# Performance work log

Measured on AMD Instinct MI355X. Metric: run time of the kernel, lower is better.

## Reference

```python
import jax, jax.numpy as jnp
import numpy as np

B, T, C, H = 256, 256, 384, 6
HS = C // H        # 64 head size
P = int(C * 0.8)   # 307 pca_dim
EPS = 1e-6


def _rmsnorm(x, scale):
    rms = jnp.sqrt(jnp.mean(x * x, axis=-1, keepdims=True) + EPS)
    return x / rms * scale


def _orth(W):
    # torch.svd returns V (not V^T); u @ v.t() == u @ vt
    u, _, vt = jnp.linalg.svd(W, full_matrices=False)
    return u @ vt


def setup_inputs() -> dict:
    key = jax.random.key(0)
    ks = jax.random.split(key, 16)
    s = 0.02
    inp = {
        'x': jax.random.normal(ks[0], (B, T, C), jnp.float32),
        'Wq': jax.random.normal(ks[1], (H, C, HS), jnp.float32) * s,
        'Wk': jax.random.normal(ks[2], (H, C, HS), jnp.float32) * s,
        'Wv': jax.random.normal(ks[3], (H, C, HS), jnp.float32) * s,
        'Wp': jax.random.normal(ks[4], (H * HS, C), jnp.float32) * s,
        'bp': jnp.zeros((C,), jnp.float32),
        'scale1': jnp.ones((C,), jnp.float32),
        'scale2': jnp.ones((C,), jnp.float32),
        'W1': jax.random.normal(ks[5], (C, P), jnp.float32) * s,
        'b1': jnp.zeros((P,), jnp.float32),
        'W2': jax.random.normal(ks[6], (P, C), jnp.float32) * s,
        'b2': jnp.zeros((C,), jnp.float32),
        'Wo_in': jax.random.normal(ks[7], (C, C), jnp.float32),
        'Wo_out': jax.random.normal(ks[8], (C, C), jnp.float32),
    }
    return inp


def reference(x, Wq, Wk, Wv, Wp, bp, scale1, scale2, W1, b1, W2, b2, Wo_in, Wo_out):
    # ln1
    h = _rmsnorm(x, scale1)                                   # [B,T,C]
    # multi-head causal self-attention (heads batched via einsum)
    q = jnp.einsum('btc,hcd->bhtd', h, Wq)                    # [B,H,T,HS]
    k = jnp.einsum('btc,hcd->bhtd', h, Wk)
    v = jnp.einsum('btc,hcd->bhtd', h, Wv)
    wei = jnp.einsum('bhtd,bhsd->bhts', q, k) * (HS ** -0.5)  # [B,H,T,T]
    causal = jnp.tril(jnp.ones((T, T), bool))
    wei = jnp.where(causal, wei, -jnp.inf)
    wei = jax.nn.softmax(wei, axis=-1)
    attn = jnp.einsum('bhts,bhsd->bhtd', wei, v)              # [B,H,T,HS]
    attn = attn.transpose(0, 2, 1, 3).reshape(B, T, H * HS)   # concat heads
    h = attn @ Wp + bp + h                                    # residual on ln1 output
    # ln2
    h = _rmsnorm(h, scale2)
    # input orthogonal transform
    h = h @ _orth(Wo_in)
    # PCA feed-forward (dropout = identity in eval)
    h = jax.nn.relu(h @ W1 + b1)
    h = h @ W2 + b2
    # output orthogonal transform + residual on ff output
    out = h @ _orth(Wo_out) + h
    return out
```

## Files before the change

kernel.cpp:

```cpp
#include <hip/hip_runtime.h>

typedef unsigned short u16;
typedef unsigned int   u32;
typedef short s16x8 __attribute__((ext_vector_type(8)));
typedef float f32x4 __attribute__((ext_vector_type(4)));

static __device__ __forceinline__ float bf2f(u16 v){ return __uint_as_float(((u32)v)<<16); }
static __device__ __forceinline__ u16 f2bf(float f){
  u32 u = __float_as_uint(f);
  u32 r = (u + 0x7fffu + ((u>>16)&1u)) >> 16;
  return (u16)r;
}
static __device__ __forceinline__ float cvt(float v){ return v; }
static __device__ __forceinline__ float cvt(u16 v){ return bf2f(v); }
static __device__ __forceinline__ void stv(float* p, float v){ *p = v; }
static __device__ __forceinline__ void stv(u16* p, float v){ *p = f2bf(v); }

static __device__ __forceinline__ void ld2(const float* p, float& a, float& b){
  float2 t = *(const float2*)p; a=t.x; b=t.y;
}
static __device__ __forceinline__ void ld2(const u16* p, float& a, float& b){
  u32 t = *(const u32*)p; a = __uint_as_float(t<<16); b = __uint_as_float(t & 0xffff0000u);
}
static __device__ __forceinline__ void st2(float* p, float a, float b){
  float2 t; t.x=a; t.y=b; *(float2*)p = t;
}
static __device__ __forceinline__ void st2(u16* p, float a, float b){
  *(u32*)p = ((u32)f2bf(a)) | (((u32)f2bf(b))<<16);
}

static __device__ __forceinline__ void gload16(const u16* g, u16* l){
  __builtin_amdgcn_global_load_lds(
      (const __attribute__((address_space(1))) u32*)(const void*)g,
      (__attribute__((address_space(3))) u32*)(void*)l, 16, 0, 0);
}

template<typename TI, typename TO>
__global__ __launch_bounds__(256) void rms_k(const TI* __restrict__ X,
                                             const float* __restrict__ scale,
                                             TO* __restrict__ O)
{
  int row = blockIdx.x*4 + (threadIdx.x>>6);
  int lane = threadIdx.x&63;
  const TI* xr = X + (size_t)row*384;
  float v[6]; float ss = 0.f;
#pragma unroll
  for(int i=0;i<3;i++){
    ld2(xr + 2*lane + 128*i, v[2*i], v[2*i+1]);
    ss += v[2*i]*v[2*i] + v[2*i+1]*v[2*i+1];
  }
#pragma unroll
  for(int off=32; off>0; off>>=1) ss += __shfl_down(ss, off, 64);
  ss = __shfl(ss, 0, 64);
  float r = rsqrtf(ss*(1.0f/384.0f)+1e-6f);
  TO* orow = O + (size_t)row*384;
#pragma unroll
  for(int i=0;i<3;i++){
    int c = 2*lane + 128*i;
    st2(orow + c, v[2*i]*r*scale[c], v[2*i+1]*r*scale[c+1]);
  }
}

__global__ __launch_bounds__(256) void tcast_k(const float* __restrict__ In, long isz,
                                               u16* __restrict__ Out, long osz,
                                               int Rr, int Cc, int ldo)
{
  __shared__ float t[32][33];
  const int z = blockIdx.z;
  const float* I = In + (long)z*isz;
  u16* Oz = Out + (long)z*osz;
  const int r0 = blockIdx.x*32, c0 = blockIdx.y*32;
  const int tx = threadIdx.x&31, ty = threadIdx.x>>5;
#pragma unroll
  for(int rr=ty; rr<32; rr+=8){
    int r = r0+rr, c = c0+tx;
    t[rr][tx] = (r<Rr && c<Cc) ? I[(size_t)r*Cc + c] : 0.f;
  }
  __syncthreads();
#pragma unroll
  for(int cc=ty; cc<32; cc+=8){
    int c = c0+cc, r = r0+tx;
    if(c<Cc && r<ldo) Oz[(size_t)c*ldo + r] = f2bf(t[tx][cc]);
  }
}

template<int NF, typename TC, typename TR>
__global__ __launch_bounds__(256,3) void mgemm2_k(
    const u16* __restrict__ A, int lda,
    const u16* __restrict__ Bt, int ldb,
    TC* __restrict__ C, long cs_hi, int cs_lo, int csz,
    const TR* __restrict__ R,
    const float* __restrict__ bias,
    int N, int Nstore, int K, float beta, int relu, int nby)
{
  constexpr int BN = NF*32;
  __shared__ __align__(16) u16 As[128*64];
  __shared__ __align__(16) u16 Bs[BN*64];
  const int d = blockIdx.x;
  const int xcd = d&7, slot = d>>3;
  const int bm = xcd*64 + slot/nby;
  const int bn = slot - (slot/nby)*nby;
  const int m0 = bm*128, n0 = bn*BN;
  const int tid = threadIdx.x;
  const int w = tid>>6, lane = tid&63;
  const int g4 = lane>>4, l16 = lane&15;
  const int wr = w>>1, wc = w&1;
  const int srow = lane>>3;
  const int sc8  = ((lane&7) ^ srow) * 8;
  const u16* aSrc[4];
#pragma unroll
  for(int i=0;i<4;i++)
    aSrc[i] = A + (size_t)(m0 + 8*(w+4*i) + srow)*lda + sc8;
  const u16* bSrc[NF];
#pragma unroll
  for(int i=0;i<NF;i++)
    bSrc[i] = Bt + (size_t)(n0 + 8*(w+4*i) + srow)*ldb + sc8;

  f32x4 fz = {0.f,0.f,0.f,0.f};
  f32x4 acc[4][NF];
#pragma unroll
  for(int i=0;i<4;i++)
#pragma unroll
    for(int j=0;j<NF;j++) acc[i][j]=fz;

  const int sxor = l16&7;
  for(int k0=0;k0<K;k0+=64){
#pragma unroll
    for(int i=0;i<4;i++)  gload16(aSrc[i] + k0, &As[(w+4*i)*512]);
#pragma unroll
    for(int i=0;i<NF;i++) gload16(bSrc[i] + k0, &Bs[(w+4*i)*512]);
    __syncthreads();
#pragma unroll
    for(int ks=0; ks<2; ++ks){
      s16x8 av[4];
#pragma unroll
      for(int mf=0;mf<4;mf++){
        int Rr_ = wr*64 + mf*16 + l16;
        av[mf] = *(const s16x8*)&As[Rr_*64 + 8*((ks*4+g4) ^ sxor)];
      }
      s16x8 bv[NF];
#pragma unroll
      for(int nf=0;nf<NF;nf++){
        int Rn = wc*(NF*16) + nf*16 + l16;
        bv[nf] = *(const s16x8*)&Bs[Rn*64 + 8*((ks*4+g4) ^ sxor)];
      }
#pragma unroll
      for(int mf=0;mf<4;mf++)
#pragma unroll
        for(int nf=0;nf<NF;nf++)
          acc[mf][nf] = __builtin_amdgcn_mfma_f32_16x16x32_bf16(av[mf], bv[nf], acc[mf][nf], 0,0,0);
    }
    __syncthreads();
  }
#pragma unroll
  for(int mf=0;mf<4;mf++)
#pragma unroll
    for(int i=0;i<4;i++){
      int m = m0 + wr*64 + mf*16 + g4*4 + i;
      long rowoff = (long)(m>>8)*cs_hi + (long)(m&255)*cs_lo;
#pragma unroll
      for(int nf=0;nf<NF;nf++){
        int gn = n0 + wc*(NF*16) + nf*16 + l16;
        if(gn < Nstore){
          long addr = rowoff + (long)(gn>>6)*csz + (gn&63);
          float v = 0.f;
          if(gn < N){
            v = acc[mf][nf][i];
            if(R)    v += beta*cvt(R[addr]);
            if(bias) v += bias[gn];
            if(relu) v  = fmaxf(v, 0.f);
          }
          stv(C + addr, v);
        }
      }
    }
}

__global__ __launch_bounds__(256,2) void mattn_k(const u16* __restrict__ QKV,
                                                 u16* __restrict__ O)
{
  __shared__ __align__(16) u16 Ks[64*64];
  __shared__ __align__(16) u16 Vts[64*64];
  __shared__ __align__(16) u16 Ps[4*4096];
  const int bh = blockIdx.x;
  const int b = bh/6, h = bh - b*6;
  const u16* Qb = QKV + (size_t)bh*49152;
  const u16* Kb = Qb + 16384;
  const u16* Vb = Qb + 32768;
  const int tid = threadIdx.x;
  const int w = tid>>6, lane = tid&63;
  const int g4 = lane>>4, l16 = lane&15;
  char* PB = (char*)&Ps[w*4096];
  const int swz = (l16&7)<<4;

  s16x8 qf[4][2];
#pragma unroll
  for(int mi=0;mi<4;mi++)
#pragma unroll
    for(int ks=0;ks<2;ks++)
      qf[mi][ks] = *(const s16x8*)(Qb + (size_t)(w*64 + mi*16 + l16)*64 + ks*32 + g4*8);

  f32x4 fzv = {0.f,0.f,0.f,0.f};
  f32x4 o[4][4];
#pragma unroll
  for(int mf=0;mf<4;mf++)
#pragma unroll
    for(int df=0;df<4;df++) o[mf][df]=fzv;
  float mrun[4], lrun[4];
#pragma unroll
  for(int mi=0;mi<4;mi++){ mrun[mi]=-1e30f; lrun[mi]=0.f; }

  for(int st=0; st<4; ++st){
    if(st) __syncthreads();
#pragma unroll
    for(int it=0; it<2; ++it){
      int c = tid + 256*it;
      int s = c>>3, d0 = (c&7)*8;
      uint4 ld = *(const uint4*)(Kb + (size_t)(st*64+s)*64 + d0);
      int byte = s*128 + d0*2; byte ^= (s&7)<<4;
      *(uint4*)((char*)Ks + byte) = ld;
    }
#pragma unroll
    for(int it=0; it<2; ++it){
      int c = tid + 256*it;
      int s = c&63, d0 = (c>>6)*8;
      uint4 ld = *(const uint4*)(Vb + (size_t)(st*64+s)*64 + d0);
#pragma unroll
      for(int jj=0; jj<4; ++jj){
        u32 ww = (jj==0)?ld.x:(jj==1)?ld.y:(jj==2)?ld.z:ld.w;
        int d = d0 + 2*jj;
        int byte0 = d*128 + s*2;     byte0 ^= (d&7)<<4;
        int byte1 = (d+1)*128 + s*2; byte1 ^= ((d+1)&7)<<4;
        *(u16*)((char*)Vts + byte0) = (u16)(ww & 0xffffu);
        *(u16*)((char*)Vts + byte1) = (u16)(ww >> 16);
      }
    }
    __syncthreads();
    if(w < st) continue;

    f32x4 sc[4][4];
#pragma unroll
    for(int sf=0; sf<4; ++sf){
      int row = sf*16 + l16;
      s16x8 kf0 = *(const s16x8*)((char*)Ks + ((row*128 + g4*16) ^ swz));
      s16x8 kf1 = *(const s16x8*)((char*)Ks + ((row*128 + 64 + g4*16) ^ swz));
#pragma unroll
      for(int mi=0; mi<4; ++mi){
        f32x4 t = __builtin_amdgcn_mfma_f32_16x16x32_bf16(kf0, qf[mi][0], fzv, 0,0,0);
        sc[sf][mi] = __builtin_amdgcn_mfma_f32_16x16x32_bf16(kf1, qf[mi][1], t, 0,0,0);
      }
    }
    float alpha[4];
#pragma unroll
    for(int mi=0; mi<4; ++mi){
      int mloc = mi*16 + l16;
      float rmax = -3.0e38f;
#pragma unroll
      for(int sf=0; sf<4; ++sf)
#pragma unroll
        for(int i=0;i<4;i++){
          float vv = sc[sf][mi][i]*0.125f;
          if(st==w && (sf*16 + g4*4 + i) > mloc) vv = -1e30f;
          sc[sf][mi][i] = vv;
          rmax = fmaxf(rmax, vv);
        }
      rmax = fmaxf(rmax, __shfl_xor(rmax, 16, 64));
      rmax = fmaxf(rmax, __shfl_xor(rmax, 32, 64));
      float mnew = fmaxf(mrun[mi], rmax);
      float al = __expf(mrun[mi] - mnew);
      mrun[mi] = mnew;
      float ls = 0.f;
#pragma unroll
      for(int sf=0; sf<4; ++sf){
        float p0 = __expf(sc[sf][mi][0]-mnew);
        float p1 = __expf(sc[sf][mi][1]-mnew);
        float p2 = __expf(sc[sf][mi][2]-mnew);
        float p3 = __expf(sc[sf][mi][3]-mnew);
        ls += p0+p1+p2+p3;
        ushort4 pk; pk.x=f2bf(p0); pk.y=f2bf(p1); pk.z=f2bf(p2); pk.w=f2bf(p3);
        int byte = mloc*128 + sf*32 + g4*8; byte ^= (l16&7)<<4;
        *(ushort4*)(PB + byte) = pk;
      }
      ls += __shfl_xor(ls, 16, 64);
      ls += __shfl_xor(ls, 32, 64);
      lrun[mi] = lrun[mi]*al + ls;
      alpha[mi] = al;
    }
#pragma unroll
    for(int mf=0; mf<4; ++mf)
#pragma unroll
      for(int i=0;i<4;i++){
        float at = __shfl(alpha[mf], g4*4 + i, 64);
#pragma unroll
        for(int df=0; df<4; ++df) o[mf][df][i] *= at;
      }
    s16x8 vbf[4][2];
#pragma unroll
    for(int df=0; df<4; ++df){
      int row = df*16 + l16;
      vbf[df][0] = *(const s16x8*)((char*)Vts + ((row*128 + g4*16) ^ swz));
      vbf[df][1] = *(const s16x8*)((char*)Vts + ((row*128 + 64 + g4*16) ^ swz));
    }
#pragma unroll
    for(int mf=0; mf<4; ++mf){
      int row = mf*16 + l16;
      s16x8 pa0 = *(const s16x8*)(PB + ((row*128 + g4*16) ^ swz));
      s16x8 pa1 = *(const s16x8*)(PB + ((row*128 + 64 + g4*16) ^ swz));
#pragma unroll
      for(int df=0; df<4; ++df){
        f32x4 t = __builtin_amdgcn_mfma_f32_16x16x32_bf16(pa0, vbf[df][0], o[mf][df], 0,0,0);
        o[mf][df] = __builtin_amdgcn_mfma_f32_16x16x32_bf16(pa1, vbf[df][1], t, 0,0,0);
      }
    }
  }
#pragma unroll
  for(int mf=0; mf<4; ++mf)
#pragma unroll
    for(int i=0;i<4;i++){
      float lt = __shfl(lrun[mf], g4*4 + i, 64);
      float rl = 1.f/lt;
      u16* orow = O + ((size_t)(b*256 + w*64 + mf*16 + g4*4 + i))*384 + h*64;
#pragma unroll
      for(int df=0; df<4; ++df)
        orow[df*16 + l16] = f2bf(o[mf][df][i]*rl);
    }
}

__global__ __launch_bounds__(256) void fpart_k(const float* __restrict__ W0,
                                               const float* __restrict__ W1,
                                               float* __restrict__ part)
{
  int b = blockIdx.x; int z = b/24, seg = b - z*24;
  const float* W = (z ? W1 : W0) + seg*6144;
  int tid = threadIdx.x;
  float s = 0.f;
  for(int i=tid;i<6144;i+=256){ float v=W[i]; s+=v*v; }
#pragma unroll
  for(int off=32; off>0; off>>=1) s += __shfl_down(s, off, 64);
  __shared__ float red[4];
  if((tid&63)==0) red[tid>>6]=s;
  __syncthreads();
  if(tid==0) part[b] = red[0]+red[1]+red[2]+red[3];
}

__global__ __launch_bounds__(64) void fcomb_k(const float* __restrict__ part,
                                              float* __restrict__ invb)
{
  int lane = threadIdx.x;
  float v = 0.f;
  if(lane < 24) v = part[lane];
  else if(lane >= 32 && lane < 56) v = part[lane - 8];
#pragma unroll
  for(int off=1; off<32; off<<=1) v += __shfl_xor(v, off, 64);
  if(lane==0)  invb[0] = rsqrtf(v);
  if(lane==32) invb[1] = rsqrtf(v);
}

__global__ __launch_bounds__(256) void nsinit_k(const float* __restrict__ W0,
                                                const float* __restrict__ W1,
                                                const float* __restrict__ invb,
                                                u16* __restrict__ XB)
{
  int b = blockIdx.x; int z = b/24, p = b - z*24, cp0 = p*16;
  const float* W = z ? W1 : W0;
  float inv = invb[z];
  u16* base = XB + (size_t)z*589824;
  u16* xh = base;            u16* xl = base + 147456;
  u16* th = base + 294912;   u16* tl = base + 442368;
  int tid = threadIdx.x;
  for(int idx=tid; idx<6144; idx+=256){
    int r = idx>>4, j = idx&15;
    float v = W[r*384 + cp0 + j]*inv;
    u16 hh = f2bf(v);
    xh[p*6144 + idx] = hh;
    xl[p*6144 + idx] = f2bf(v - bf2f(hh));
  }
  for(int idx=tid; idx<6144; idx+=256){
    int j = idx/384, r = idx - j*384;
    float v = W[(cp0+j)*384 + r]*inv;
    u16 hh = f2bf(v);
    th[p*6144 + r*16 + j] = hh;
    tl[p*6144 + r*16 + j] = f2bf(v - bf2f(hh));
  }
}

static __device__ __forceinline__ void ns_mm(
    const u16* __restrict__ Agh, const u16* __restrict__ Agl,
    u16* AhL, u16* AlL, const u16* BThL, const u16* BTlL,
    int tid, f32x4 acc[4])
{
  const int w = tid>>6, lane = tid&63, g4 = lane>>4, l16 = lane&15;
  const int o0 = (tid>>1)*24 + (tid&1)*8;
  const int o1 = o0 + 4608;
  const s16x8 z8 = {0,0,0,0,0,0,0,0};
  f32x4 fz = {0.f,0.f,0.f,0.f};
#pragma unroll
  for(int i=0;i<4;i++) acc[i]=fz;
  {
    uint4 h0 = *(const uint4*)(Agh + tid*8);
    uint4 h1 = *(const uint4*)(Agh + (384+tid)*8);
    uint4 l0 = *(const uint4*)(Agl + tid*8);
    uint4 l1 = *(const uint4*)(Agl + (384+tid)*8);
    *(uint4*)&AhL[o0] = h0; *(uint4*)&AhL[o1] = h1;
    *(uint4*)&AlL[o0] = l0; *(uint4*)&AlL[o1] = l1;
  }
  __syncthreads();
  for(int c=0;c<24;c++){
    uint4 nh0, nh1, nl0, nl1;
    if(c<23){
      const u16* ph = Agh + (c+1)*6144;
      const u16* pl = Agl + (c+1)*6144;
      nh0 = *(const uint4*)(ph + tid*8);
      nh1 = *(const uint4*)(ph + (384+tid)*8);
      nl0 = *(const uint4*)(pl + tid*8);
      nl1 = *(const uint4*)(pl + (384+tid)*8);
    }
    s16x8 bh = z8, bl = z8;
    if(g4<2){
      bh = *(const s16x8*)&BThL[l16*392 + c*16 + g4*8];
      bl = *(const s16x8*)&BTlL[l16*392 + c*16 + g4*8];
    }
#pragma unroll
    for(int tt=0;tt<4;tt++){
      int rb = 64*w + 16*tt + l16;
      s16x8 ah = z8, al = z8;
      if(g4<2){
        ah = *(const s16x8*)&AhL[rb*24 + g4*8];
        al = *(const s16x8*)&AlL[rb*24 + g4*8];
      }
      acc[tt] = __builtin_amdgcn_mfma_f32_16x16x32_bf16(ah, bh, acc[tt], 0,0,0);
      acc[tt] = __builtin_amdgcn_mfma_f32_16x16x32_bf16(ah, bl, acc[tt], 0,0,0);
      acc[tt] = __builtin_amdgcn_mfma_f32_16x16x32_bf16(al, bh, acc[tt], 0,0,0);
    }
    __syncthreads();
    if(c<23){
      *(uint4*)&AhL[o0] = nh0; *(uint4*)&AhL[o1] = nh1;
      *(uint4*)&AlL[o0] = nl0; *(uint4*)&AlL[o1] = nl1;
      __syncthreads();
    }
  }
}

__global__ __launch_bounds__(384) void nsit_k(u16* __restrict__ XB,
                                              u16* __restrict__ QT,
                                              int it, int niter, int nq)
{
  __shared__ __align__(16) u16 AhL[384*24];
  __shared__ __align__(16) u16 AlL[384*24];
  __shared__ __align__(16) u16 BTh[16*392];
  __shared__ __align__(16) u16 BTl[16*392];
  const int blk = blockIdx.x;
  const int z = blk/24, p = blk - z*24, cp0 = p*16;
  const int tid = threadIdx.x;
  const int w = tid>>6, lane = tid&63, g4 = lane>>4, l16 = lane&15;
  const int rs = it&1, ws2 = rs^1;
  const u16* bin  = XB + (size_t)rs*1179648  + (size_t)z*589824;
  u16*       bout = XB + (size_t)ws2*1179648 + (size_t)z*589824;
  const u16* Xh  = bin;            const u16* Xl  = bin + 147456;
  const u16* Th  = bin + 294912;   const u16* Tl  = bin + 442368;

  {
    const u16* sh = Xh + p*6144;
    const u16* sl = Xl + p*6144;
    for(int i=tid; i<768; i+=384){
      int k = i>>1, n0 = (i&1)*8;
      uint4 vh = *(const uint4*)(sh + i*8);
      uint4 vl = *(const uint4*)(sl + i*8);
#pragma unroll
      for(int j=0;j<8;j++){
        BTh[(n0+j)*392 + k] = ((u16*)&vh)[j];
        BTl[(n0+j)*392 + k] = ((u16*)&vl)[j];
      }
    }
  }
  __syncthreads();

  const bool quint = (it < nq);
  f32x4 acc[4], gsv[4];

  ns_mm(Th, Tl, AhL, AlL, BTh, BTl, tid, acc);
  if(quint){
#pragma unroll
    for(int tt=0;tt<4;tt++){
      gsv[tt] = acc[tt];
      int m0 = 64*w + 16*tt + g4*4;
      ushort4 h4, l4;
#pragma unroll
      for(int i=0;i<4;i++){
        float v = acc[tt][i];
        u16 hh = f2bf(v);
        ((u16*)&h4)[i]=hh; ((u16*)&l4)[i]=f2bf(v - bf2f(hh));
      }
      *(ushort4*)&BTh[l16*392 + m0] = h4;
      *(ushort4*)&BTl[l16*392 + m0] = l4;
    }
    __syncthreads();
    ns_mm(Xh, Xl, AhL, AlL, BTh, BTl, tid, acc);
#pragma unroll
    for(int tt=0;tt<4;tt++){
      int m0 = 64*w + 16*tt + g4*4;
      ushort4 h4, l4;
#pragma unroll
      for(int i=0;i<4;i++){
        float v = acc[tt][i];
        u16 hh = f2bf(v);
        ((u16*)&h4)[i]=hh; ((u16*)&l4)[i]=f2bf(v - bf2f(hh));
      }
      *(ushort4*)&BTh[l16*392 + m0] = h4;
      *(ushort4*)&BTl[l16*392 + m0] = l4;
    }
    __syncthreads();
    ns_mm(Th, Tl, AhL, AlL, BTh, BTl, tid, acc);
    __syncthreads();
#pragma unroll
    for(int tt=0;tt<4;tt++){
      int m0 = 64*w + 16*tt + g4*4;
      ushort4 h4, l4;
#pragma unroll
      for(int i=0;i<4;i++){
        float v = fmaf(2.0315f, acc[tt][i], -4.7750f*(gsv[tt][i]))
                + ((m0+i)==(cp0+l16) ? 3.4445f : 0.f);
        u16 hh = f2bf(v);
        ((u16*)&h4)[i]=hh; ((u16*)&l4)[i]=f2bf(v - bf2f(hh));
      }
      *(ushort4*)&BTh[l16*392 + m0] = h4;
      *(ushort4*)&BTl[l16*392 + m0] = l4;
    }
    __syncthreads();
  } else {
#pragma unroll
    for(int tt=0;tt<4;tt++){
      int m0 = 64*w + 16*tt + g4*4;
      ushort4 h4, l4;
#pragma unroll
      for(int i=0;i<4;i++){
        float v = -0.5f*acc[tt][i] + ((m0+i)==(cp0+l16) ? 1.5f : 0.f);
        u16 hh = f2bf(v);
        ((u16*)&h4)[i]=hh; ((u16*)&l4)[i]=f2bf(v - bf2f(hh));
      }
      *(ushort4*)&BTh[l16*392 + m0] = h4;
      *(ushort4*)&BTl[l16*392 + m0] = l4;
    }
    __syncthreads();
  }
  ns_mm(Xh, Xl, AhL, AlL, BTh, BTl, tid, acc);

  if(it == niter-1){
    u16* q = QT + (size_t)z*147456 + (size_t)(cp0+l16)*384;
#pragma unroll
    for(int tt=0;tt<4;tt++){
      int m0 = 64*w + 16*tt + g4*4;
      ushort4 h4;
#pragma unroll
      for(int i=0;i<4;i++) ((u16*)&h4)[i] = f2bf(acc[tt][i]);
      *(ushort4*)&q[m0] = h4;
    }
  } else {
    u16* oXh = bout + p*6144;            u16* oXl = bout + 147456 + p*6144;
    u16* oTh = bout + 294912;            u16* oTl = bout + 442368;
#pragma unroll
    for(int tt=0;tt<4;tt++){
      int m0 = 64*w + 16*tt + g4*4;
      ushort4 h4, l4;
#pragma unroll
      for(int i=0;i<4;i++){
        float v = acc[tt][i];
        u16 hh = f2bf(v);
        ((u16*)&h4)[i]=hh; ((u16*)&l4)[i]=f2bf(v - bf2f(hh));
        oXh[(m0+i)*16 + l16] = hh;
        oXl[(m0+i)*16 + l16] = ((u16*)&l4)[i];
      }
      size_t to = (size_t)(4*w+tt)*6144 + (size_t)(cp0+l16)*16 + g4*4;
      *(ushort4*)&oTh[to] = h4;
      *(ushort4*)&oTl[to] = l4;
    }
  }
}

extern "C" void kernel_launch(void* const* d_in, const int* in_sizes, int n_in,
                              void* d_out, int out_size, void* d_ws, size_t ws_size,
                              hipStream_t stream)
{
  const float* x      = (const float*)d_in[0];
  const float* Wq     = (const float*)d_in[1];
  const float* Wk     = (const float*)d_in[2];
  const float* Wv     = (const float*)d_in[3];
  const float* Wp     = (const float*)d_in[4];
  const float* bp     = (const float*)d_in[5];
  const float* scale1 = (const float*)d_in[6];
  const float* scale2 = (const float*)d_in[7];
  const float* W1     = (const float*)d_in[8];
  const float* b1     = (const float*)d_in[9];
  const float* W2     = (const float*)d_in[10];
  const float* b2     = (const float*)d_in[11];
  const float* Wo_in  = (const float*)d_in[12];
  const float* Wo_out = (const float*)d_in[13];

  char* ws = (char*)d_ws;
  u16* XB   = (u16*)(ws + 0);
  u16* Wqkv = (u16*)(ws + 4719104L);
  u16* WpT  = (u16*)(ws + 5603840L);
  u16* W1T  = (u16*)(ws + 5898752L);
  u16* W2T  = (u16*)(ws + 6134528L);
  u16* QT   = (u16*)(ws + 6380288L);
  float* part = (float*)(ws + 6970112L);
  float* invb = (float*)(ws + 6970496L);
  u16* h1b  = (u16*)(ws + 8388608L);
  u16* qkvb = (u16*)(ws + 58720256L);
  u16* atb  = (u16*)(ws + 209715200L);
  u16* h2b = qkvb;
  u16* h3b = qkvb + 25165824L;
  u16* h4b = qkvb + 50331648L;
  u16* h5b = atb;
  u16* h6b = h1b;

  tcast_k<<<dim3(12, 2,6),256,0,stream>>>(Wq,24576L, Wqkv,        73728L, 384, 64,384);
  tcast_k<<<dim3(12, 2,6),256,0,stream>>>(Wk,24576L, Wqkv+24576L, 73728L, 384, 64,384);
  tcast_k<<<dim3(12, 2,6),256,0,stream>>>(Wv,24576L, Wqkv+49152L, 73728L, 384, 64,384);
  tcast_k<<<dim3(12,12,1),256,0,stream>>>(Wp,0L,     WpT,0L,     384,384,384);
  tcast_k<<<dim3(12,10,1),256,0,stream>>>(W1,0L,     W1T,0L,     384,307,384);
  tcast_k<<<dim3(10,12,1),256,0,stream>>>(W2,0L,     W2T,0L,     307,384,320);

  const int NITER = 15, NQ = 10;
  fpart_k<<<48,256,0,stream>>>(Wo_in, Wo_out, part);
  fcomb_k<<<1,64,0,stream>>>(part, invb);
  nsinit_k<<<48,256,0,stream>>>(Wo_in, Wo_out, invb, XB);
  for(int it=0; it<NITER; ++it)
    nsit_k<<<48,384,0,stream>>>(XB, QT, it, NITER, NQ);

  rms_k<float,u16><<<16384,256,0,stream>>>(x, scale1, h1b);
  mgemm2_k<6,u16,float><<<3072,256,0,stream>>>(
      h1b,384,  Wqkv,384,
      qkvb, 294912L,64,16384,
      (const float*)nullptr, nullptr,
      1152,1152,384, 0.f,0, 6);
  mattn_k<<<1536,256,0,stream>>>(qkvb, atb);
  mgemm2_k<6,u16,u16><<<1024,256,0,stream>>>(
      atb,384,  WpT,384,
      h2b, 98304L,384,64,
      h1b, bp,
      384,384,384, 1.f,0, 2);
  rms_k<u16,u16><<<16384,256,0,stream>>>(h2b, scale2, h3b);
  mgemm2_k<6,u16,float><<<1024,256,0,stream>>>(
      h3b,384,  QT,384,
      h4b, 98304L,384,64,
      (const float*)nullptr, nullptr,
      384,384,384, 0.f,0, 2);
  mgemm2_k<5,u16,float><<<1024,256,0,stream>>>(
      h4b,384,  W1T,384,
      h5b, 81920L,320,64,
      (const float*)nullptr, b1,
      307,320,384, 0.f,1, 2);
  mgemm2_k<6,u16,float><<<1024,256,0,stream>>>(
      h5b,320,  W2T,320,
      h6b, 98304L,384,64,
      (const float*)nullptr, b2,
      384,384,320, 0.f,0, 2);
  mgemm2_k<6,float,u16><<<1024,256,0,stream>>>(
      h6b,384,  QT+147456,384,
      (float*)d_out, 98304L,384,64,
      h6b, nullptr,
      384,384,384, 1.f,0, 2);

  (void)in_sizes; (void)n_in; (void)ws_size; (void)out_size;
}
```

Before: 1.595 ms.

## Fuse Newton-Schulz launches into cooperative kernel and shrink GEMM N-tiles

Merges the Frobenius-norm partial reduction, the combine step, the NS init and all 15 Newton-Schulz iteration launches into one cooperative kernel that uses grid.sync between phases, removing about 17 small launches. Separately, every mgemm2 instance moves from 6- or 5-fragment N tiles to 2-fragment tiles, with grid sizes adjusted, and the launch bounds go from 3 to 4 blocks per SM. The smaller tiles raise occupancy and block count but cut A-tile reuse and add redundant A loads. Cooperative launch also requires that all 48 blocks can be resident at once.

```diff
diff --git a/kernel.cpp b/kernel.cpp
--- a/kernel.cpp
+++ b/kernel.cpp
@@ -1,4 +1,7 @@
 #include <hip/hip_runtime.h>
+#include <hip/hip_cooperative_groups.h>
+
+namespace cg = cooperative_groups;
 
 typedef unsigned short u16;
 typedef unsigned int   u32;
@@ -85,7 +88,7 @@
 }
 
 template<int NF, typename TC, typename TR>
-__global__ __launch_bounds__(256,3) void mgemm2_k(
+__global__ __launch_bounds__(256,4) void mgemm2_k(
     const u16* __restrict__ A, int lda,
     const u16* __restrict__ Bt, int ldb,
     TC* __restrict__ C, long cs_hi, int cs_lo, int csz,
@@ -326,64 +329,6 @@
     }
 }
 
-__global__ __launch_bounds__(256) void fpart_k(const float* __restrict__ W0,
-                                               const float* __restrict__ W1,
-                                               float* __restrict__ part)
-{
-  int b = blockIdx.x; int z = b/24, seg = b - z*24;
-  const float* W = (z ? W1 : W0) + seg*6144;
-  int tid = threadIdx.x;
-  float s = 0.f;
-  for(int i=tid;i<6144;i+=256){ float v=W[i]; s+=v*v; }
-#pragma unroll
-  for(int off=32; off>0; off>>=1) s += __shfl_down(s, off, 64);
-  __shared__ float red[4];
-  if((tid&63)==0) red[tid>>6]=s;
-  __syncthreads();
-  if(tid==0) part[b] = red[0]+red[1]+red[2]+red[3];
-}
-
-__global__ __launch_bounds__(64) void fcomb_k(const float* __restrict__ part,
-                                              float* __restrict__ invb)
-{
-  int lane = threadIdx.x;
-  float v = 0.f;
-  if(lane < 24) v = part[lane];
-  else if(lane >= 32 && lane < 56) v = part[lane - 8];
-#pragma unroll
-  for(int off=1; off<32; off<<=1) v += __shfl_xor(v, off, 64);
-  if(lane==0)  invb[0] = rsqrtf(v);
-  if(lane==32) invb[1] = rsqrtf(v);
-}
-
-__global__ __launch_bounds__(256) void nsinit_k(const float* __restrict__ W0,
-                                                const float* __restrict__ W1,
-                                                const float* __restrict__ invb,
-                                                u16* __restrict__ XB)
-{
-  int b = blockIdx.x; int z = b/24, p = b - z*24, cp0 = p*16;
-  const float* W = z ? W1 : W0;
-  float inv = invb[z];
-  u16* base = XB + (size_t)z*589824;
-  u16* xh = base;            u16* xl = base + 147456;
-  u16* th = base + 294912;   u16* tl = base + 442368;
-  int tid = threadIdx.x;
-  for(int idx=tid; idx<6144; idx+=256){
-    int r = idx>>4, j = idx&15;
-    float v = W[r*384 + cp0 + j]*inv;
-    u16 hh = f2bf(v);
-    xh[p*6144 + idx] = hh;
-    xl[p*6144 + idx] = f2bf(v - bf2f(hh));
-  }
-  for(int idx=tid; idx<6144; idx+=256){
-    int j = idx/384, r = idx - j*384;
-    float v = W[(cp0+j)*384 + r]*inv;
-    u16 hh = f2bf(v);
-    th[p*6144 + r*16 + j] = hh;
-    tl[p*6144 + r*16 + j] = f2bf(v - bf2f(hh));
-  }
-}
-
 static __device__ __forceinline__ void ns_mm(
     const u16* __restrict__ Agh, const u16* __restrict__ Agl,
     u16* AhL, u16* AlL, const u16* BThL, const u16* BTlL,
@@ -441,138 +386,187 @@
   }
 }
 
-__global__ __launch_bounds__(384) void nsit_k(u16* __restrict__ XB,
-                                              u16* __restrict__ QT,
-                                              int it, int niter, int nq)
+__global__ __launch_bounds__(384,1) void ns_all_k(const float* __restrict__ W0,
+                                                  const float* __restrict__ W1,
+                                                  float* __restrict__ part,
+                                                  u16* __restrict__ XB,
+                                                  u16* __restrict__ QT,
+                                                  int niter, int nq)
 {
+  cg::grid_group grid = cg::this_grid();
   __shared__ __align__(16) u16 AhL[384*24];
   __shared__ __align__(16) u16 AlL[384*24];
   __shared__ __align__(16) u16 BTh[16*392];
   __shared__ __align__(16) u16 BTl[16*392];
+  __shared__ float red[6];
   const int blk = blockIdx.x;
   const int z = blk/24, p = blk - z*24, cp0 = p*16;
   const int tid = threadIdx.x;
   const int w = tid>>6, lane = tid&63, g4 = lane>>4, l16 = lane&15;
-  const int rs = it&1, ws2 = rs^1;
-  const u16* bin  = XB + (size_t)rs*1179648  + (size_t)z*589824;
-  u16*       bout = XB + (size_t)ws2*1179648 + (size_t)z*589824;
-  const u16* Xh  = bin;            const u16* Xl  = bin + 147456;
-  const u16* Th  = bin + 294912;   const u16* Tl  = bin + 442368;
+  const float* W = z ? W1 : W0;
 
   {
-    const u16* sh = Xh + p*6144;
-    const u16* sl = Xl + p*6144;
-    for(int i=tid; i<768; i+=384){
-      int k = i>>1, n0 = (i&1)*8;
-      uint4 vh = *(const uint4*)(sh + i*8);
-      uint4 vl = *(const uint4*)(sl + i*8);
-#pragma unroll
-      for(int j=0;j<8;j++){
-        BTh[(n0+j)*392 + k] = ((u16*)&vh)[j];
-        BTl[(n0+j)*392 + k] = ((u16*)&vl)[j];
-      }
-    }
-  }
-  __syncthreads();
-
-  const bool quint = (it < nq);
-  f32x4 acc[4], gsv[4];
-
-  ns_mm(Th, Tl, AhL, AlL, BTh, BTl, tid, acc);
-  if(quint){
-#pragma unroll
-    for(int tt=0;tt<4;tt++){
-      gsv[tt] = acc[tt];
-      int m0 = 64*w + 16*tt + g4*4;
-      ushort4 h4, l4;
-#pragma unroll
-      for(int i=0;i<4;i++){
-        float v = acc[tt][i];
-        u16 hh = f2bf(v);
-        ((u16*)&h4)[i]=hh; ((u16*)&l4)[i]=f2bf(v - bf2f(hh));
-      }
-      *(ushort4*)&BTh[l16*392 + m0] = h4;
-      *(ushort4*)&BTl[l16*392 + m0] = l4;
-    }
+    float s = 0.f;
+    const float* seg = W + p*6144;
+    for(int i=tid;i<6144;i+=384){ float v=seg[i]; s+=v*v; }
+#pragma unroll
+    for(int off=32; off>0; off>>=1) s += __shfl_down(s, off, 64);
+    if(lane==0) red[w]=s;
     __syncthreads();
+    if(tid==0){
+      float a = red[0]+red[1]+red[2]+red[3]+red[4]+red[5];
+      part[blk]=a;
+    }
+  }
+  grid.sync();
+  {
+    float a=0.f;
+#pragma unroll 4
+    for(int i=0;i<24;i++) a += part[z*24+i];
+    float inv = rsqrtf(a);
+    u16* base = XB + (size_t)z*589824;
+    u16* xh = base;            u16* xl = base + 147456;
+    u16* th = base + 294912;   u16* tl = base + 442368;
+    for(int idx=tid; idx<6144; idx+=384){
+      int r = idx>>4, j = idx&15;
+      float v = W[r*384 + cp0 + j]*inv;
+      u16 hh = f2bf(v);
+      xh[p*6144 + idx] = hh;
+      xl[p*6144 + idx] = f2bf(v - bf2f(hh));
+    }
+    for(int idx=tid; idx<6144; idx+=384){
+      int j = idx/384, r = idx - j*384;
+      float v = W[(cp0+j)*384 + r]*inv;
+      u16 hh = f2bf(v);
+      th[p*6144 + r*16 + j] = hh;
+      tl[p*6144 + r*16 + j] = f2bf(v - bf2f(hh));
+    }
+  }
+  grid.sync();
+
+  for(int it=0; it<niter; ++it){
+    const int rs = it&1;
+    const u16* bin  = XB + (size_t)rs*1179648     + (size_t)z*589824;
+    u16*       bout = XB + (size_t)(rs^1)*1179648 + (size_t)z*589824;
+    const u16* Xh  = bin;            const u16* Xl  = bin + 147456;
+    const u16* Th  = bin + 294912;   const u16* Tl  = bin + 442368;
+
+    {
+      const u16* sh = Xh + p*6144;
+      const u16* sl = Xl + p*6144;
+      for(int i=tid; i<768; i+=384){
+        int k = i>>1, n0 = (i&1)*8;
+        uint4 vh = *(const uint4*)(sh + i*8);
+        uint4 vl = *(const uint4*)(sl + i*8);
+#pragma unroll
+        for(int j=0;j<8;j++){
+          BTh[(n0+j)*392 + k] = ((u16*)&vh)[j];
+          BTl[(n0+j)*392 + k] = ((u16*)&vl)[j];
+        }
+      }
+    }
+    __syncthreads();
+
+    const bool quint = (it < nq);
+    f32x4 acc[4], gsv[4];
+
+    ns_mm(Th, Tl, AhL, AlL, BTh, BTl, tid, acc);
+    if(quint){
+#pragma unroll
+      for(int tt=0;tt<4;tt++){
+        gsv[tt] = acc[tt];
+        int m0 = 64*w + 16*tt + g4*4;
+        ushort4 h4, l4;
+#pragma unroll
+        for(int i=0;i<4;i++){
+          float v = acc[tt][i];
+          u16 hh = f2bf(v);
+          ((u16*)&h4)[i]=hh; ((u16*)&l4)[i]=f2bf(v - bf2f(hh));
+        }
+        *(ushort4*)&BTh[l16*392 + m0] = h4;
+        *(ushort4*)&BTl[l16*392 + m0] = l4;
+      }
+      __syncthreads();
+      ns_mm(Xh, Xl, AhL, AlL, BTh, BTl, tid, acc);
+#pragma unroll
+      for(int tt=0;tt<4;tt++){
+        int m0 = 64*w + 16*tt + g4*4;
+        ushort4 h4, l4;
+#pragma unroll
+        for(int i=0;i<4;i++){
+          float v = acc[tt][i];
+          u16 hh = f2bf(v);
+          ((u16*)&h4)[i]=hh; ((u16*)&l4)[i]=f2bf(v - bf2f(hh));
+        }
+        *(ushort4*)&BTh[l16*392 + m0] = h4;
+        *(ushort4*)&BTl[l16*392 + m0] = l4;
+      }
+      __syncthreads();
+      ns_mm(Th, Tl, AhL, AlL, BTh, BTl, tid, acc);
+      __syncthreads();
+#pragma unroll
+      for(int tt=0;tt<4;tt++){
+        int m0 = 64*w + 16*tt + g4*4;
+        ushort4 h4, l4;
+#pragma unroll
+        for(int i=0;i<4;i++){
+          float v = fmaf(2.0315f, acc[tt][i], -4.7750f*(gsv[tt][i]))
+                  + ((m0+i)==(cp0+l16) ? 3.4445f : 0.f);
+          u16 hh = f2bf(v);
+          ((u16*)&h4)[i]=hh; ((u16*)&l4)[i]=f2bf(v - bf2f(hh));
+        }
+        *(ushort4*)&BTh[l16*392 + m0] = h4;
+        *(ushort4*)&BTl[l16*392 + m0] = l4;
+      }
+      __syncthreads();
+    } else {
+#pragma unroll
+      for(int tt=0;tt<4;tt++){
+        int m0 = 64*w + 16*tt + g4*4;
+        ushort4 h4, l4;
+#pragma unroll
+        for(int i=0;i<4;i++){
+          float v = -0.5f*acc[tt][i] + ((m0+i)==(cp0+l16) ? 1.5f : 0.f);
+          u16 hh = f2bf(v);
+          ((u16*)&h4)[i]=hh; ((u16*)&l4)[i]=f2bf(v - bf2f(hh));
+        }
+        *(ushort4*)&BTh[l16*392 + m0] = h4;
+        *(ushort4*)&BTl[l16*392 + m0] = l4;
+      }
+      __syncthreads();
+    }
     ns_mm(Xh, Xl, AhL, AlL, BTh, BTl, tid, acc);
-#pragma unroll
-    for(int tt=0;tt<4;tt++){
-      int m0 = 64*w + 16*tt + g4*4;
-      ushort4 h4, l4;
-#pragma unroll
-      for(int i=0;i<4;i++){
-        float v = acc[tt][i];
-        u16 hh = f2bf(v);
-        ((u16*)&h4)[i]=hh; ((u16*)&l4)[i]=f2bf(v - bf2f(hh));
-      }
-      *(ushort4*)&BTh[l16*392 + m0] = h4;
-      *(ushort4*)&BTl[l16*392 + m0] = l4;
-    }
-    __syncthreads();
-    ns_mm(Th, Tl, AhL, AlL, BTh, BTl, tid, acc);
-    __syncthreads();
-#pragma unroll
-    for(int tt=0;tt<4;tt++){
-      int m0 = 64*w + 16*tt + g4*4;
-      ushort4 h4, l4;
-#pragma unroll
-      for(int i=0;i<4;i++){
-        float v = fmaf(2.0315f, acc[tt][i], -4.7750f*(gsv[tt][i]))
-                + ((m0+i)==(cp0+l16) ? 3.4445f : 0.f);
-        u16 hh = f2bf(v);
-        ((u16*)&h4)[i]=hh; ((u16*)&l4)[i]=f2bf(v - bf2f(hh));
-      }
-      *(ushort4*)&BTh[l16*392 + m0] = h4;
-      *(ushort4*)&BTl[l16*392 + m0] = l4;
-    }
-    __syncthreads();
-  } else {
-#pragma unroll
-    for(int tt=0;tt<4;tt++){
-      int m0 = 64*w + 16*tt + g4*4;
-      ushort4 h4, l4;
-#pragma unroll
-      for(int i=0;i<4;i++){
-        float v = -0.5f*acc[tt][i] + ((m0+i)==(cp0+l16) ? 1.5f : 0.f);
-        u16 hh = f2bf(v);
-        ((u16*)&h4)[i]=hh; ((u16*)&l4)[i]=f2bf(v - bf2f(hh));
-      }
-      *(ushort4*)&BTh[l16*392 + m0] = h4;
-      *(ushort4*)&BTl[l16*392 + m0] = l4;
-    }
-    __syncthreads();
-  }
-  ns_mm(Xh, Xl, AhL, AlL, BTh, BTl, tid, acc);
-
-  if(it == niter-1){
-    u16* q = QT + (size_t)z*147456 + (size_t)(cp0+l16)*384;
-#pragma unroll
-    for(int tt=0;tt<4;tt++){
-      int m0 = 64*w + 16*tt + g4*4;
-      ushort4 h4;
-#pragma unroll
-      for(int i=0;i<4;i++) ((u16*)&h4)[i] = f2bf(acc[tt][i]);
-      *(ushort4*)&q[m0] = h4;
-    }
-  } else {
-    u16* oXh = bout + p*6144;            u16* oXl = bout + 147456 + p*6144;
-    u16* oTh = bout + 294912;            u16* oTl = bout + 442368;
-#pragma unroll
-    for(int tt=0;tt<4;tt++){
-      int m0 = 64*w + 16*tt + g4*4;
-      ushort4 h4, l4;
-#pragma unroll
-      for(int i=0;i<4;i++){
-        float v = acc[tt][i];
-        u16 hh = f2bf(v);
-        ((u16*)&h4)[i]=hh; ((u16*)&l4)[i]=f2bf(v - bf2f(hh));
-        oXh[(m0+i)*16 + l16] = hh;
-        oXl[(m0+i)*16 + l16] = ((u16*)&l4)[i];
-      }
-      size_t to = (size_t)(4*w+tt)*6144 + (size_t)(cp0+l16)*16 + g4*4;
-      *(ushort4*)&oTh[to] = h4;
-      *(ushort4*)&oTl[to] = l4;
+
+    if(it == niter-1){
+      u16* q = QT + (size_t)z*147456 + (size_t)(cp0+l16)*384;
+#pragma unroll
+      for(int tt=0;tt<4;tt++){
+        int m0 = 64*w + 16*tt + g4*4;
+        ushort4 h4;
+#pragma unroll
+        for(int i=0;i<4;i++) ((u16*)&h4)[i] = f2bf(acc[tt][i]);
+        *(ushort4*)&q[m0] = h4;
+      }
+    } else {
+      u16* oXh = bout + p*6144;            u16* oXl = bout + 147456 + p*6144;
+      u16* oTh = bout + 294912;            u16* oTl = bout + 442368;
+#pragma unroll
+      for(int tt=0;tt<4;tt++){
+        int m0 = 64*w + 16*tt + g4*4;
+        ushort4 h4, l4;
+#pragma unroll
+        for(int i=0;i<4;i++){
+          float v = acc[tt][i];
+          u16 hh = f2bf(v);
+          ((u16*)&h4)[i]=hh; ((u16*)&l4)[i]=f2bf(v - bf2f(hh));
+          oXh[(m0+i)*16 + l16] = hh;
+          oXl[(m0+i)*16 + l16] = ((u16*)&l4)[i];
+        }
+        size_t to = (size_t)(4*w+tt)*6144 + (size_t)(cp0+l16)*16 + g4*4;
+        *(ushort4*)&oTh[to] = h4;
+        *(ushort4*)&oTl[to] = l4;
+      }
+      grid.sync();
     }
   }
 }
@@ -604,7 +598,6 @@
   u16* W2T  = (u16*)(ws + 6134528L);
   u16* QT   = (u16*)(ws + 6380288L);
   float* part = (float*)(ws + 6970112L);
-  float* invb = (float*)(ws + 6970496L);
   u16* h1b  = (u16*)(ws + 8388608L);
   u16* qkvb = (u16*)(ws + 58720256L);
   u16* atb  = (u16*)(ws + 209715200L);
@@ -621,46 +614,49 @@
   tcast_k<<<dim3(12,10,1),256,0,stream>>>(W1,0L,     W1T,0L,     384,307,384);
   tcast_k<<<dim3(10,12,1),256,0,stream>>>(W2,0L,     W2T,0L,     307,384,320);
 
-  const int NITER = 15, NQ = 10;
-  fpart_k<<<48,256,0,stream>>>(Wo_in, Wo_out, part);
-  fcomb_k<<<1,64,0,stream>>>(part, invb);
-  nsinit_k<<<48,256,0,stream>>>(Wo_in, Wo_out, invb, XB);
-  for(int it=0; it<NITER; ++it)
-    nsit_k<<<48,384,0,stream>>>(XB, QT, it, NITER, NQ);
+  {
+    const float* a0 = Wo_in; const float* a1 = Wo_out;
+    float* pp = part; u16* px = XB; u16* pq = QT;
+    int ni = 15, nq = 10;
+    void* nsargs[] = { (void*)&a0, (void*)&a1, (void*)&pp, (void*)&px,
+                       (void*)&pq, (void*)&ni, (void*)&nq };
+    hipLaunchCooperativeKernel((const void*)&ns_all_k, dim3(48), dim3(384),
+                               nsargs, 0u, stream);
+  }
 
   rms_k<float,u16><<<16384,256,0,stream>>>(x, scale1, h1b);
-  mgemm2_k<6,u16,float><<<3072,256,0,stream>>>(
+  mgemm2_k<2,u16,float><<<9216,256,0,stream>>>(
       h1b,384,  Wqkv,384,
       qkvb, 294912L,64,16384,
       (const float*)nullptr, nullptr,
-      1152,1152,384, 0.f,0, 6);
+      1152,1152,384, 0.f,0, 18);
   mattn_k<<<1536,256,0,stream>>>(qkvb, atb);
-  mgemm2_k<6,u16,u16><<<1024,256,0,stream>>>(
+  mgemm2_k<2,u16,u16><<<3072,256,0,stream>>>(
       atb,384,  WpT,384,
       h2b, 98304L,384,64,
       h1b, bp,
-      384,384,384, 1.f,0, 2);
+      384,384,384, 1.f,0, 6);
   rms_k<u16,u16><<<16384,256,0,stream>>>(h2b, scale2, h3b);
-  mgemm2_k<6,u16,float><<<1024,256,0,stream>>>(
+  mgemm2_k<2,u16,float><<<3072,256,0,stream>>>(
       h3b,384,  QT,384,
       h4b, 98304L,384,64,
       (const float*)nullptr, nullptr,
-      384,384,384, 0.f,0, 2);
-  mgemm2_k<5,u16,float><<<1024,256,0,stream>>>(
+      384,384,384, 0.f,0, 6);
+  mgemm2_k<2,u16,float><<<2560,256,0,stream>>>(
       h4b,384,  W1T,384,
       h5b, 81920L,320,64,
       (const float*)nullptr, b1,
-      307,320,384, 0.f,1, 2);
-  mgemm2_k<6,u16,float><<<1024,256,0,stream>>>(
+      307,320,384, 0.f,1, 5);
+  mgemm2_k<2,u16,float><<<3072,256,0,stream>>>(
       h5b,320,  W2T,320,
       h6b, 98304L,384,64,
       (const float*)nullptr, b2,
-      384,384,320, 0.f,0, 2);
-  mgemm2_k<6,float,u16><<<1024,256,0,stream>>>(
+      384,384,320, 0.f,0, 6);
+  mgemm2_k<2,float,u16><<<3072,256,0,stream>>>(
       h6b,384,  QT+147456,384,
       (float*)d_out, 98304L,384,64,
       h6b, nullptr,
-      384,384,384, 1.f,0, 2);
+      384,384,384, 1.f,0, 6);
 
   (void)in_sizes; (void)n_in; (void)ws_size; (void)out_size;
 }
```

After: 1.569 ms. Within noise of the previous version (-1.6%).
